# Optimization experiments

Hardware: AMD Instinct MI355X
Metric: run time of the kernel (lower is better)

## Reference

```python
import jax, jax.numpy as jnp
import numpy as np

EMBED_DIM = 2048
NUM_HEADS = 16
B, L = 1, 4096


def setup_inputs() -> dict:
    key = jax.random.key(0)
    ks = jax.random.split(key, 6)
    s = 1.0 / np.sqrt(EMBED_DIM)
    return {
        "hidden_states": jax.random.normal(ks[0], (B, L, EMBED_DIM), jnp.float32),
        "Wq": jax.random.normal(ks[1], (EMBED_DIM, EMBED_DIM), jnp.float32) * s,
        "bq": jnp.zeros((EMBED_DIM,), jnp.float32),
        "Wk": jax.random.normal(ks[2], (EMBED_DIM, EMBED_DIM), jnp.float32) * s,
        "bk": jnp.zeros((EMBED_DIM,), jnp.float32),
        "Wv": jax.random.normal(ks[3], (EMBED_DIM, EMBED_DIM), jnp.float32) * s,
        "bv": jnp.zeros((EMBED_DIM,), jnp.float32),
        "Wo": jax.random.normal(ks[4], (EMBED_DIM, EMBED_DIM), jnp.float32) * s,
        "bo": jnp.zeros((EMBED_DIM,), jnp.float32),
        "is_causal": 1,
    }


def reference(hidden_states, Wq, bq, Wk, bk, Wv, bv, Wo, bo, is_causal):
    Bc, Lc, D = hidden_states.shape
    H = NUM_HEADS
    Dh = D // H
    scale = Dh ** (-0.5)

    def proj(W, b):
        # torch Linear: x @ W.T + b; reshape to [B, H, L, Dh]
        y = jnp.einsum('bld,ed->ble', hidden_states, W) + b
        return y.reshape(Bc, Lc, H, Dh).transpose(0, 2, 1, 3)

    q = proj(Wq, bq)
    k = proj(Wk, bk)
    v = proj(Wv, bv)

    scores = jnp.einsum('bhqd,bhkd->bhqk', q, k) * scale  # [B,H,L,L]
    if is_causal:
        causal = jnp.triu(jnp.ones((Lc, Lc), dtype=bool), k=1)
        scores = jnp.where(causal, -jnp.inf, scores)
    w = jax.nn.softmax(scores, axis=-1)
    attn = jnp.einsum('bhqk,bhkd->bhqd', w, v)
    attn = attn.transpose(0, 2, 1, 3).reshape(Bc, Lc, D)
    return jnp.einsum('bld,ed->ble', attn, Wo) + bo
```

## Files before the change

kernel.cpp:

```cpp
#include <hip/hip_runtime.h>
#include <hip/hip_bf16.h>

typedef unsigned short u16;
typedef __attribute__((ext_vector_type(8))) short short8;
typedef __attribute__((ext_vector_type(4))) float f32x4;

#define L 4096
#define DMODEL 2048
#define NHEADS 16
#define DHEAD 128
#define QSCALE (0.08838834764831845f * 1.44269504088896340f)

__device__ __forceinline__ u16 f2bf(float f){
  union { float f; unsigned int i; } v; v.f = f;
  unsigned int u = v.i;
  u += 0x7fffu + ((u >> 16) & 1u);
  return (u16)(u >> 16);
}

__device__ __forceinline__ unsigned int cvtpk(float lo, float hi){
  unsigned int d;
  asm("v_cvt_pk_bf16_f32 %0, %1, %2" : "=v"(d) : "v"(lo), "v"(hi));
  return d;
}

__global__ void cast_kernel(const float* __restrict__ in, u16* __restrict__ out, int n){
  int stride = gridDim.x * blockDim.x * 4;
  for (int j = (blockIdx.x * blockDim.x + threadIdx.x) * 4; j < n; j += stride){
    float4 f = *reinterpret_cast<const float4*>(in + j);
    ushort4 o;
    o.x = f2bf(f.x); o.y = f2bf(f.y); o.z = f2bf(f.z); o.w = f2bf(f.w);
    *reinterpret_cast<ushort4*>(out + j) = o;
  }
}

__global__ void cast_w4_kernel(const float* __restrict__ w0, const float* __restrict__ w1,
                               const float* __restrict__ w2, const float* __restrict__ w3,
                               u16* __restrict__ o0, u16* __restrict__ o1,
                               u16* __restrict__ o2, u16* __restrict__ o3){
  const float* in = (blockIdx.y == 0) ? w0 : (blockIdx.y == 1) ? w1 : (blockIdx.y == 2) ? w2 : w3;
  u16* out = (blockIdx.y == 0) ? o0 : (blockIdx.y == 1) ? o1 : (blockIdx.y == 2) ? o2 : o3;
  const int n = DMODEL * DMODEL;
  int stride = gridDim.x * blockDim.x * 4;
  for (int j = (blockIdx.x * blockDim.x + threadIdx.x) * 4; j < n; j += stride){
    float4 f = *reinterpret_cast<const float4*>(in + j);
    ushort4 o;
    o.x = f2bf(f.x); o.y = f2bf(f.y); o.z = f2bf(f.z); o.w = f2bf(f.w);
    *reinterpret_cast<ushort4*>(out + j) = o;
  }
}

__device__ __forceinline__ void gl_lds16(void* lds, const void* g){
  __builtin_amdgcn_global_load_lds(
      (const __attribute__((address_space(1))) unsigned int*)g,
      (__attribute__((address_space(3))) unsigned int*)lds, 16, 0, 0);
}

#define GBUF (24576)

template<int MODE>
__global__ __launch_bounds__(512, 2) void gemm_bt(const u16* __restrict__ A, const u16* __restrict__ Bw,
                                                  const float* __restrict__ bias, void* __restrict__ outp,
                                                  float cscale){
  extern __shared__ u16 gsm[];
  const int tid = threadIdx.x;
  const int wid = tid >> 6, lane = tid & 63;
  const int wm = wid >> 2, wn = wid & 3;
  const int g = lane >> 4, r = lane & 15;
  const int bx = blockIdx.x, by = blockIdx.y;

  const int srow = tid >> 3;
  const int sc = ((tid & 7) * 16) ^ ((srow & 7) << 4);
  const u16* Ag = A  + ((size_t)(bx * 256) + srow) * DMODEL + (sc >> 1);
  const u16* Bg = Bw + ((size_t)(by * 128) + srow) * DMODEL + (sc >> 1);
  const int ldsw = wid * 1024;

  f32x4 acc[8][2];
  #pragma unroll
  for (int m = 0; m < 8; ++m){ acc[m][0] = (f32x4){0,0,0,0}; acc[m][1] = (f32x4){0,0,0,0}; }

  const int NK = DMODEL / 64;

  auto STAGE = [&](int b, int tk){
    char* ab = (char*)(gsm + b * GBUF);
    char* bb = (char*)(gsm + b * GBUF + 16384);
    const int ke = tk * 64;
    #pragma unroll
    for (int i = 0; i < 4; ++i)
      gl_lds16(ab + i * 8192 + ldsw, (const char*)(Ag + (size_t)i * 64 * DMODEL + ke));
    #pragma unroll
    for (int i = 0; i < 2; ++i)
      gl_lds16(bb + i * 8192 + ldsw, (const char*)(Bg + (size_t)i * 64 * DMODEL + ke));
  };

  STAGE(0, 0); STAGE(1, 1); STAGE(2, 2);

  int cur = 0;
  for (int t = 0; t < NK; ++t){
    if (t < NK - 2)      asm volatile("s_waitcnt vmcnt(12)" ::: "memory");
    else if (t == NK - 2) asm volatile("s_waitcnt vmcnt(6)"  ::: "memory");
    else                  asm volatile("s_waitcnt vmcnt(0)"  ::: "memory");
    __builtin_amdgcn_sched_barrier(0);
    __builtin_amdgcn_s_barrier();
    __builtin_amdgcn_sched_barrier(0);

    const char* ab = (const char*)(gsm + cur * GBUF);
    const char* bb = (const char*)(gsm + cur * GBUF + 16384);

    short8 af[8][2], bf[2][2];
    #pragma unroll
    for (int mt = 0; mt < 8; ++mt){
      const int ar = wm * 128 + mt * 16 + r;
      #pragma unroll
      for (int ks = 0; ks < 2; ++ks)
        af[mt][ks] = *reinterpret_cast<const short8*>(
            ab + ar * 128 + ((ks * 64 + g * 16) ^ ((ar & 7) << 4)));
    }
    #pragma unroll
    for (int nt = 0; nt < 2; ++nt){
      const int br = wn * 32 + nt * 16 + r;
      #pragma unroll
      for (int ks = 0; ks < 2; ++ks)
        bf[nt][ks] = *reinterpret_cast<const short8*>(
            bb + br * 128 + ((ks * 64 + g * 16) ^ ((br & 7) << 4)));
    }
    asm volatile("s_waitcnt lgkmcnt(0)" ::: "memory");
    __builtin_amdgcn_sched_barrier(0);
    __builtin_amdgcn_s_barrier();
    __builtin_amdgcn_sched_barrier(0);

    if (t + 3 < NK) STAGE(cur, t + 3);

    __builtin_amdgcn_s_setprio(1);
    #pragma unroll
    for (int mt = 0; mt < 8; ++mt)
      #pragma unroll
      for (int nt = 0; nt < 2; ++nt)
        #pragma unroll
        for (int ks = 0; ks < 2; ++ks)
          acc[mt][nt] = __builtin_amdgcn_mfma_f32_16x16x32_bf16(af[mt][ks], bf[nt][ks], acc[mt][nt], 0, 0, 0);
    __builtin_amdgcn_s_setprio(0);

    cur = (cur == 2) ? 0 : cur + 1;
  }

  #pragma unroll
  for (int nt = 0; nt < 2; ++nt){
    const int col = by * 128 + wn * 32 + nt * 16 + r;
    const float bv = bias[col];
    #pragma unroll
    for (int mt = 0; mt < 8; ++mt){
      #pragma unroll
      for (int qi = 0; qi < 4; ++qi){
        const int row = bx * 256 + wm * 128 + mt * 16 + g * 4 + qi;
        float c = acc[mt][nt][qi] + bv;
        if (MODE == 0){
          ((u16*)outp)[(size_t)(col >> 7) * (L * DHEAD) + (size_t)row * DHEAD + (col & 127)] = f2bf(c * cscale);
        } else if (MODE == 1){
          ((u16*)outp)[(size_t)(col >> 7) * (DHEAD * L) + (size_t)(col & 127) * L + row] = f2bf(c);
        } else {
          ((float*)outp)[(size_t)row * DMODEL + col] = c;
        }
      }
    }
  }
}


__device__ __forceinline__ void stage_K64(u16* buf, const u16* Kh, int kv0, int wid, int lane){
  #pragma unroll
  for (int i = 0; i < 4; ++i){
    int ib = (wid * 4 + i) * 1024;
    int off = ib + lane * 16;
    int row = off >> 8;
    int c = off & 255;
    int sc = c ^ ((row & 7) << 4);
    gl_lds16((char*)buf + ib, (const char*)(Kh + (size_t)(kv0 + row) * DHEAD) + sc);
  }
}

__device__ __forceinline__ void stage_V64(u16* buf, const u16* Vh, int kv0, int wid, int lane){
  #pragma unroll
  for (int i = 0; i < 4; ++i){
    int ib = (wid * 4 + i) * 1024;
    int off = ib + lane * 16;
    int row = off >> 7;
    int c = off & 127;
    int sc = c ^ ((row & 7) << 4);
    gl_lds16((char*)buf + ib, (const char*)(Vh + (size_t)row * L + kv0) + sc);
  }
}

__device__ __forceinline__ void sm_F(f32x4 (&s)[4], float &l, bool dg, int qrow,
                                     int kv0, int g, int r, char* Pw, int prow0){
  if (dg){
    #pragma unroll
    for (int cb = 0; cb < 4; ++cb){
      int kvb = kv0 + cb * 16 + g * 4;
      #pragma unroll
      for (int e = 0; e < 4; ++e)
        if (kvb + e > qrow) s[cb][e] = -1e30f;
    }
  }
  float rs = 0.f;
  uint2 pkv[4];
  #pragma unroll
  for (int cb = 0; cb < 4; ++cb){
    float p0 = __builtin_amdgcn_exp2f(s[cb][0]);
    float p1 = __builtin_amdgcn_exp2f(s[cb][1]);
    float p2 = __builtin_amdgcn_exp2f(s[cb][2]);
    float p3 = __builtin_amdgcn_exp2f(s[cb][3]);
    rs += (p0 + p1) + (p2 + p3);
    pkv[cb].x = cvtpk(p0, p1);
    pkv[cb].y = cvtpk(p2, p3);
  }
  rs += __shfl_xor(rs, 16);
  rs += __shfl_xor(rs, 32);
  l += rs;
  const int row = prow0 + r;
  char* base = Pw + row * 128;
  #pragma unroll
  for (int cb = 0; cb < 4; ++cb)
    *reinterpret_cast<uint2*>(base + ((cb * 32 + g * 8) ^ ((row & 7) << 4))) = pkv[cb];
}

__global__ __launch_bounds__(256, 2) void attn_kernel(const u16* __restrict__ Q, const u16* __restrict__ Km,
                                                      const u16* __restrict__ Vt, u16* __restrict__ Ob,
                                                      const int* __restrict__ is_causal_p){
  extern __shared__ u16 smem[];
  u16* Ks  = smem;
  u16* Vsm = smem + 16384;
  u16* Ps  = smem + 32768;

  const int lane = threadIdx.x & 63, wid = threadIdx.x >> 6;
  const int g = lane >> 4, r = lane & 15;

  int lg = (blockIdx.x & 7) * 64 + (blockIdx.x >> 3);
  int head = lg >> 5;
  int raw = lg & 31;
  int j = (head & 1) ? (31 - raw) : raw;
  const int jA = j, jB = 63 - j;
  const int causal = *is_causal_p;
  const int nt = causal ? (jB + 1) : 64;

  const u16* Qh = Q  + (size_t)head * L * DHEAD;
  const u16* Kh = Km + (size_t)head * L * DHEAD;
  const u16* Vh = Vt + (size_t)head * DHEAD * L;
  char* Pw = (char*)(Ps + wid * 2048);

  const int rowA = 64 * jA + wid * 16;
  const int rowB = 64 * jB + wid * 16;

  short8 qf[2][4];
  #pragma unroll
  for (int kb = 0; kb < 4; ++kb){
    qf[0][kb] = *reinterpret_cast<const short8*>(&Qh[(size_t)(rowA + r) * DHEAD + kb * 32 + g * 8]);
    qf[1][kb] = *reinterpret_cast<const short8*>(&Qh[(size_t)(rowB + r) * DHEAD + kb * 32 + g * 8]);
  }

  f32x4 o[2][8];
  #pragma unroll
  for (int m = 0; m < 2; ++m)
    #pragma unroll
    for (int db = 0; db < 8; ++db) o[m][db] = (f32x4){0.f, 0.f, 0.f, 0.f};
  float lA = 0.f, lB = 0.f;

  stage_K64(Ks,  Kh, 0, wid, lane);
  stage_V64(Vsm, Vh, 0, wid, lane);

  for (int t = 0; t < nt; ++t){
    const int kv0 = t * 64;
    const bool actA = (!causal) || (t <= jA);
    const bool dgA = causal && (t == jA);
    const bool dgB = causal && (t == jB);

    if (t + 1 < nt){
      stage_K64(Ks  + ((t + 1) & 1) * 8192, Kh, kv0 + 64, wid, lane);
      stage_V64(Vsm + ((t + 1) & 1) * 8192, Vh, kv0 + 64, wid, lane);
      asm volatile("s_waitcnt vmcnt(8)" ::: "memory");
    } else {
      asm volatile("s_waitcnt vmcnt(0)" ::: "memory");
    }
    __builtin_amdgcn_sched_barrier(0);
    __builtin_amdgcn_s_barrier();
    __builtin_amdgcn_sched_barrier(0);

    const char* Kb = (const char*)(Ks  + (t & 1) * 8192);
    const char* Vb = (const char*)(Vsm + (t & 1) * 8192);

    f32x4 s[2][4];
    #pragma unroll
    for (int m = 0; m < 2; ++m)
      #pragma unroll
      for (int cb = 0; cb < 4; ++cb) s[m][cb] = (f32x4){-16.f, -16.f, -16.f, -16.f};
    __builtin_amdgcn_s_setprio(1);
    #pragma unroll
    for (int cb = 0; cb < 4; ++cb){
      const int rr = cb * 16 + r;
      short8 kf[4];
      #pragma unroll
      for (int kb = 0; kb < 4; ++kb)
        kf[kb] = *reinterpret_cast<const short8*>(
            Kb + rr * 256 + ((kb * 64 + g * 16) ^ ((rr & 7) << 4)));
      if (actA){
        #pragma unroll
        for (int kb = 0; kb < 4; ++kb)
          s[0][cb] = __builtin_amdgcn_mfma_f32_16x16x32_bf16(kf[kb], qf[0][kb], s[0][cb], 0, 0, 0);
      }
      #pragma unroll
      for (int kb = 0; kb < 4; ++kb)
        s[1][cb] = __builtin_amdgcn_mfma_f32_16x16x32_bf16(kf[kb], qf[1][kb], s[1][cb], 0, 0, 0);
    }
    __builtin_amdgcn_s_setprio(0);

    if (actA) sm_F(s[0], lA, dgA, rowA + r, kv0, g, r, Pw, 0);
    sm_F(s[1], lB, dgB, rowB + r, kv0, g, r, Pw, 16);

    asm volatile("s_waitcnt lgkmcnt(0)" ::: "memory");
    __builtin_amdgcn_sched_barrier(0);

    __builtin_amdgcn_s_setprio(1);
    #pragma unroll
    for (int st = 0; st < 2; ++st){
      short8 pa0, pa1;
      if (actA)
        pa0 = *reinterpret_cast<const short8*>(
            Pw + r * 128 + ((st * 64 + g * 16) ^ ((r & 7) << 4)));
      pa1 = *reinterpret_cast<const short8*>(
          Pw + (16 + r) * 128 + ((st * 64 + g * 16) ^ ((r & 7) << 4)));
      #pragma unroll
      for (int db = 0; db < 8; ++db){
        const int rv = db * 16 + r;
        short8 vf = *reinterpret_cast<const short8*>(
            Vb + rv * 128 + ((st * 32 + g * 8) * 2 ^ ((rv & 7) << 4)));
        if (actA)
          o[0][db] = __builtin_amdgcn_mfma_f32_16x16x32_bf16(pa0, vf, o[0][db], 0, 0, 0);
        o[1][db] = __builtin_amdgcn_mfma_f32_16x16x32_bf16(pa1, vf, o[1][db], 0, 0, 0);
      }
    }
    __builtin_amdgcn_s_setprio(0);
    __builtin_amdgcn_sched_barrier(0);
    __builtin_amdgcn_s_barrier();
    __builtin_amdgcn_sched_barrier(0);
  }

  #pragma unroll
  for (int m = 0; m < 2; ++m){
    const int rbase = m ? rowB : rowA;
    const float lv = m ? lB : lA;
    float lb[4];
    #pragma unroll
    for (int qi = 0; qi < 4; ++qi) lb[qi] = __shfl(lv, g * 4 + qi);
    #pragma unroll
    for (int db = 0; db < 8; ++db)
      #pragma unroll
      for (int qi = 0; qi < 4; ++qi){
        float val = o[m][db][qi] / lb[qi];
        int qrow = rbase + g * 4 + qi;
        Ob[(size_t)qrow * DMODEL + head * DHEAD + db * 16 + r] = f2bf(val);
      }
  }
}

extern "C" void kernel_launch(void* const* d_in, const int* in_sizes, int n_in,
                              void* d_out, int out_size, void* d_ws, size_t ws_size,
                              hipStream_t stream){
  const float* X  = (const float*)d_in[0];
  const float* Wq = (const float*)d_in[1];
  const float* bq = (const float*)d_in[2];
  const float* Wk = (const float*)d_in[3];
  const float* bk = (const float*)d_in[4];
  const float* Wv = (const float*)d_in[5];
  const float* bv = (const float*)d_in[6];
  const float* Wo = (const float*)d_in[7];
  const float* bo = (const float*)d_in[8];
  const int*   isc = (const int*)d_in[9];

  char* ws = (char*)d_ws;
  u16* Xb  = (u16*)(ws);
  u16* Qb  = (u16*)(ws + 16777216);
  u16* Kb  = (u16*)(ws + 33554432);
  u16* Vtb = (u16*)(ws + 50331648);
  u16* Wqb = (u16*)(ws + 67108864);
  u16* Wkb = (u16*)(ws + 75497472);
  u16* Wvb = (u16*)(ws + 83886080);
  u16* Wob = (u16*)(ws + 92274688);
  u16* Ob  = Xb;

  (void)hipFuncSetAttribute(reinterpret_cast<const void*>(attn_kernel),
                            hipFuncAttributeMaxDynamicSharedMemorySize, 81920);
  (void)hipFuncSetAttribute(reinterpret_cast<const void*>(gemm_bt<0>),
                            hipFuncAttributeMaxDynamicSharedMemorySize, 147456);
  (void)hipFuncSetAttribute(reinterpret_cast<const void*>(gemm_bt<1>),
                            hipFuncAttributeMaxDynamicSharedMemorySize, 147456);
  (void)hipFuncSetAttribute(reinterpret_cast<const void*>(gemm_bt<2>),
                            hipFuncAttributeMaxDynamicSharedMemorySize, 147456);

  cast_kernel<<<2048, 256, 0, stream>>>(X, Xb, L * DMODEL);
  cast_w4_kernel<<<dim3(1024, 4), 256, 0, stream>>>(Wq, Wk, Wv, Wo, Wqb, Wkb, Wvb, Wob);

  dim3 gg(16, 16);
  gemm_bt<0><<<gg, 512, 147456, stream>>>(Xb, Wqb, bq, Qb, QSCALE);
  gemm_bt<0><<<gg, 512, 147456, stream>>>(Xb, Wkb, bk, Kb, 1.0f);
  gemm_bt<1><<<gg, 512, 147456, stream>>>(Xb, Wvb, bv, Vtb, 1.0f);

  attn_kernel<<<512, 256, 81920, stream>>>(Qb, Kb, Vtb, Ob, isc);

  gemm_bt<2><<<gg, 512, 147456, stream>>>(Ob, Wob, bo, d_out, 1.0f);
}
```

Measured before the change: 302.9 us.

## Merge QKV GEMMs into one launch and cut pipeline barriers

Folds the three Q/K/V projection GEMMs into one kernel with a 16x48 grid, selecting weights, bias, scale and output layout per block row, so the GPU sees one larger wave of work instead of three serial launches. Both GEMMs now use a single barrier per k-step with stage distance two over a triple buffer, instead of a second barrier before the prefetch. The attention kernel moves its single barrier to the top of each iteration after vmcnt(0), drops the trailing barrier, and issues all V fragment loads before the P loads. Fewer barriers reduce stalls but leave less load-latency slack, since the GEMM waits with vmcnt(6) and attention waits with vmcnt(0) before issuing the next prefetch.

Measured after the change: 299.7 us. No clear change (-1.1%).

```diff
diff --git a/kernel.cpp b/kernel.cpp
--- a/kernel.cpp
+++ b/kernel.cpp
@@ -58,10 +58,113 @@
 
 #define GBUF (24576)
 
-template<int MODE>
-__global__ __launch_bounds__(512, 2) void gemm_bt(const u16* __restrict__ A, const u16* __restrict__ Bw,
-                                                  const float* __restrict__ bias, void* __restrict__ outp,
-                                                  float cscale){
+__global__ __launch_bounds__(512, 2) void gemm_qkv(const u16* __restrict__ A,
+    const u16* __restrict__ Wq, const u16* __restrict__ Wk, const u16* __restrict__ Wv,
+    const float* __restrict__ bq, const float* __restrict__ bk, const float* __restrict__ bv,
+    u16* __restrict__ Qb, u16* __restrict__ Kb, u16* __restrict__ Vtb){
+  extern __shared__ u16 gsm[];
+  const int tid = threadIdx.x;
+  const int wid = tid >> 6, lane = tid & 63;
+  const int wm = wid >> 2, wn = wid & 3;
+  const int g = lane >> 4, r = lane & 15;
+  const int bx = blockIdx.x;
+  const int sel = blockIdx.y >> 4;
+  const int byl = blockIdx.y & 15;
+
+  const u16* W      = (sel == 0) ? Wq : (sel == 1) ? Wk : Wv;
+  const float* bias = (sel == 0) ? bq : (sel == 1) ? bk : bv;
+  const float cscale = (sel == 0) ? QSCALE : 1.0f;
+
+  const int srow = tid >> 3;
+  const int sc = ((tid & 7) * 16) ^ ((srow & 7) << 4);
+  const u16* Ag = A + ((size_t)(bx * 256) + srow) * DMODEL + (sc >> 1);
+  const u16* Bg = W + ((size_t)(byl * 128) + srow) * DMODEL + (sc >> 1);
+  const int ldsw = wid * 1024;
+
+  f32x4 acc[8][2];
+  #pragma unroll
+  for (int m = 0; m < 8; ++m){ acc[m][0] = (f32x4){0,0,0,0}; acc[m][1] = (f32x4){0,0,0,0}; }
+
+  const int NK = DMODEL / 64;
+
+  auto STAGE = [&](int b, int tk){
+    char* ab = (char*)(gsm + b * GBUF);
+    char* bb = (char*)(gsm + b * GBUF + 16384);
+    const int ke = tk * 64;
+    #pragma unroll
+    for (int i = 0; i < 4; ++i)
+      gl_lds16(ab + i * 8192 + ldsw, (const char*)(Ag + (size_t)i * 64 * DMODEL + ke));
+    #pragma unroll
+    for (int i = 0; i < 2; ++i)
+      gl_lds16(bb + i * 8192 + ldsw, (const char*)(Bg + (size_t)i * 64 * DMODEL + ke));
+  };
+
+  STAGE(0, 0); STAGE(1, 1);
+
+  for (int t = 0; t < NK; ++t){
+    if (t < NK - 1) asm volatile("s_waitcnt vmcnt(6)" ::: "memory");
+    else            asm volatile("s_waitcnt vmcnt(0)" ::: "memory");
+    __builtin_amdgcn_sched_barrier(0);
+    __builtin_amdgcn_s_barrier();
+    __builtin_amdgcn_sched_barrier(0);
+
+    if (t + 2 < NK) STAGE((t + 2) % 3, t + 2);
+
+    const char* ab = (const char*)(gsm + (t % 3) * GBUF);
+    const char* bb = (const char*)(gsm + (t % 3) * GBUF + 16384);
+
+    short8 af[8][2], bf[2][2];
+    #pragma unroll
+    for (int mt = 0; mt < 8; ++mt){
+      const int ar = wm * 128 + mt * 16 + r;
+      #pragma unroll
+      for (int ks = 0; ks < 2; ++ks)
+        af[mt][ks] = *reinterpret_cast<const short8*>(
+            ab + ar * 128 + ((ks * 64 + g * 16) ^ ((ar & 7) << 4)));
+    }
+    #pragma unroll
+    for (int nt = 0; nt < 2; ++nt){
+      const int br = wn * 32 + nt * 16 + r;
+      #pragma unroll
+      for (int ks = 0; ks < 2; ++ks)
+        bf[nt][ks] = *reinterpret_cast<const short8*>(
+            bb + br * 128 + ((ks * 64 + g * 16) ^ ((br & 7) << 4)));
+    }
+
+    __builtin_amdgcn_s_setprio(1);
+    #pragma unroll
+    for (int mt = 0; mt < 8; ++mt)
+      #pragma unroll
+      for (int nt = 0; nt < 2; ++nt)
+        #pragma unroll
+        for (int ks = 0; ks < 2; ++ks)
+          acc[mt][nt] = __builtin_amdgcn_mfma_f32_16x16x32_bf16(af[mt][ks], bf[nt][ks], acc[mt][nt], 0, 0, 0);
+    __builtin_amdgcn_s_setprio(0);
+  }
+
+  #pragma unroll
+  for (int nt = 0; nt < 2; ++nt){
+    const int col = byl * 128 + wn * 32 + nt * 16 + r;
+    const float bv = bias[col];
+    #pragma unroll
+    for (int mt = 0; mt < 8; ++mt){
+      #pragma unroll
+      for (int qi = 0; qi < 4; ++qi){
+        const int row = bx * 256 + wm * 128 + mt * 16 + g * 4 + qi;
+        const u16 hb = f2bf((acc[mt][nt][qi] + bv) * cscale);
+        if (sel < 2){
+          u16* outp = (sel == 0) ? Qb : Kb;
+          outp[(size_t)(col >> 7) * (L * DHEAD) + (size_t)row * DHEAD + (col & 127)] = hb;
+        } else {
+          Vtb[(size_t)(col >> 7) * (DHEAD * L) + (size_t)(col & 127) * L + row] = hb;
+        }
+      }
+    }
+  }
+}
+
+__global__ __launch_bounds__(512, 2) void gemm_o(const u16* __restrict__ A, const u16* __restrict__ W,
+                                                 const float* __restrict__ bias, float* __restrict__ outp){
   extern __shared__ u16 gsm[];
   const int tid = threadIdx.x;
   const int wid = tid >> 6, lane = tid & 63;
@@ -71,8 +174,8 @@
 
   const int srow = tid >> 3;
   const int sc = ((tid & 7) * 16) ^ ((srow & 7) << 4);
-  const u16* Ag = A  + ((size_t)(bx * 256) + srow) * DMODEL + (sc >> 1);
-  const u16* Bg = Bw + ((size_t)(by * 128) + srow) * DMODEL + (sc >> 1);
+  const u16* Ag = A + ((size_t)(bx * 256) + srow) * DMODEL + (sc >> 1);
+  const u16* Bg = W + ((size_t)(by * 128) + srow) * DMODEL + (sc >> 1);
   const int ldsw = wid * 1024;
 
   f32x4 acc[8][2];
@@ -93,19 +196,19 @@
       gl_lds16(bb + i * 8192 + ldsw, (const char*)(Bg + (size_t)i * 64 * DMODEL + ke));
   };
 
-  STAGE(0, 0); STAGE(1, 1); STAGE(2, 2);
-
-  int cur = 0;
+  STAGE(0, 0); STAGE(1, 1);
+
   for (int t = 0; t < NK; ++t){
-    if (t < NK - 2)      asm volatile("s_waitcnt vmcnt(12)" ::: "memory");
-    else if (t == NK - 2) asm volatile("s_waitcnt vmcnt(6)"  ::: "memory");
-    else                  asm volatile("s_waitcnt vmcnt(0)"  ::: "memory");
+    if (t < NK - 1) asm volatile("s_waitcnt vmcnt(6)" ::: "memory");
+    else            asm volatile("s_waitcnt vmcnt(0)" ::: "memory");
     __builtin_amdgcn_sched_barrier(0);
     __builtin_amdgcn_s_barrier();
     __builtin_amdgcn_sched_barrier(0);
 
-    const char* ab = (const char*)(gsm + cur * GBUF);
-    const char* bb = (const char*)(gsm + cur * GBUF + 16384);
+    if (t + 2 < NK) STAGE((t + 2) % 3, t + 2);
+
+    const char* ab = (const char*)(gsm + (t % 3) * GBUF);
+    const char* bb = (const char*)(gsm + (t % 3) * GBUF + 16384);
 
     short8 af[8][2], bf[2][2];
     #pragma unroll
@@ -124,12 +227,6 @@
         bf[nt][ks] = *reinterpret_cast<const short8*>(
             bb + br * 128 + ((ks * 64 + g * 16) ^ ((br & 7) << 4)));
     }
-    asm volatile("s_waitcnt lgkmcnt(0)" ::: "memory");
-    __builtin_amdgcn_sched_barrier(0);
-    __builtin_amdgcn_s_barrier();
-    __builtin_amdgcn_sched_barrier(0);
-
-    if (t + 3 < NK) STAGE(cur, t + 3);
 
     __builtin_amdgcn_s_setprio(1);
     #pragma unroll
@@ -140,8 +237,6 @@
         for (int ks = 0; ks < 2; ++ks)
           acc[mt][nt] = __builtin_amdgcn_mfma_f32_16x16x32_bf16(af[mt][ks], bf[nt][ks], acc[mt][nt], 0, 0, 0);
     __builtin_amdgcn_s_setprio(0);
-
-    cur = (cur == 2) ? 0 : cur + 1;
   }
 
   #pragma unroll
@@ -153,14 +248,7 @@
       #pragma unroll
       for (int qi = 0; qi < 4; ++qi){
         const int row = bx * 256 + wm * 128 + mt * 16 + g * 4 + qi;
-        float c = acc[mt][nt][qi] + bv;
-        if (MODE == 0){
-          ((u16*)outp)[(size_t)(col >> 7) * (L * DHEAD) + (size_t)row * DHEAD + (col & 127)] = f2bf(c * cscale);
-        } else if (MODE == 1){
-          ((u16*)outp)[(size_t)(col >> 7) * (DHEAD * L) + (size_t)(col & 127) * L + row] = f2bf(c);
-        } else {
-          ((float*)outp)[(size_t)row * DMODEL + col] = c;
-        }
+        outp[(size_t)row * DMODEL + col] = acc[mt][nt][qi] + bv;
       }
     }
   }
@@ -274,16 +362,15 @@
     const bool dgA = causal && (t == jA);
     const bool dgB = causal && (t == jB);
 
+    asm volatile("s_waitcnt vmcnt(0)" ::: "memory");
+    __builtin_amdgcn_sched_barrier(0);
+    __builtin_amdgcn_s_barrier();
+    __builtin_amdgcn_sched_barrier(0);
+
     if (t + 1 < nt){
       stage_K64(Ks  + ((t + 1) & 1) * 8192, Kh, kv0 + 64, wid, lane);
       stage_V64(Vsm + ((t + 1) & 1) * 8192, Vh, kv0 + 64, wid, lane);
-      asm volatile("s_waitcnt vmcnt(8)" ::: "memory");
-    } else {
-      asm volatile("s_waitcnt vmcnt(0)" ::: "memory");
-    }
-    __builtin_amdgcn_sched_barrier(0);
-    __builtin_amdgcn_s_barrier();
-    __builtin_amdgcn_sched_barrier(0);
+    }
 
     const char* Kb = (const char*)(Ks  + (t & 1) * 8192);
     const char* Vb = (const char*)(Vsm + (t & 1) * 8192);
@@ -316,12 +403,20 @@
     if (actA) sm_F(s[0], lA, dgA, rowA + r, kv0, g, r, Pw, 0);
     sm_F(s[1], lB, dgB, rowB + r, kv0, g, r, Pw, 16);
 
-    asm volatile("s_waitcnt lgkmcnt(0)" ::: "memory");
-    __builtin_amdgcn_sched_barrier(0);
-
     __builtin_amdgcn_s_setprio(1);
     #pragma unroll
     for (int st = 0; st < 2; ++st){
+      short8 vf[8];
+      #pragma unroll
+      for (int db = 0; db < 8; ++db){
+        const int rv = db * 16 + r;
+        vf[db] = *reinterpret_cast<const short8*>(
+            Vb + rv * 128 + (((st * 32 + g * 8) * 2) ^ ((rv & 7) << 4)));
+      }
+      if (st == 0){
+        asm volatile("s_waitcnt lgkmcnt(0)" ::: "memory");
+        __builtin_amdgcn_sched_barrier(0);
+      }
       short8 pa0, pa1;
       if (actA)
         pa0 = *reinterpret_cast<const short8*>(
@@ -330,18 +425,12 @@
           Pw + (16 + r) * 128 + ((st * 64 + g * 16) ^ ((r & 7) << 4)));
       #pragma unroll
       for (int db = 0; db < 8; ++db){
-        const int rv = db * 16 + r;
-        short8 vf = *reinterpret_cast<const short8*>(
-            Vb + rv * 128 + ((st * 32 + g * 8) * 2 ^ ((rv & 7) << 4)));
         if (actA)
-          o[0][db] = __builtin_amdgcn_mfma_f32_16x16x32_bf16(pa0, vf, o[0][db], 0, 0, 0);
-        o[1][db] = __builtin_amdgcn_mfma_f32_16x16x32_bf16(pa1, vf, o[1][db], 0, 0, 0);
+          o[0][db] = __builtin_amdgcn_mfma_f32_16x16x32_bf16(pa0, vf[db], o[0][db], 0, 0, 0);
+        o[1][db] = __builtin_amdgcn_mfma_f32_16x16x32_bf16(pa1, vf[db], o[1][db], 0, 0, 0);
       }
     }
     __builtin_amdgcn_s_setprio(0);
-    __builtin_amdgcn_sched_barrier(0);
-    __builtin_amdgcn_s_barrier();
-    __builtin_amdgcn_sched_barrier(0);
   }
 
   #pragma unroll
@@ -389,22 +478,17 @@
 
   (void)hipFuncSetAttribute(reinterpret_cast<const void*>(attn_kernel),
                             hipFuncAttributeMaxDynamicSharedMemorySize, 81920);
-  (void)hipFuncSetAttribute(reinterpret_cast<const void*>(gemm_bt<0>),
+  (void)hipFuncSetAttribute(reinterpret_cast<const void*>(gemm_qkv),
                             hipFuncAttributeMaxDynamicSharedMemorySize, 147456);
-  (void)hipFuncSetAttribute(reinterpret_cast<const void*>(gemm_bt<1>),
-                            hipFuncAttributeMaxDynamicSharedMemorySize, 147456);
-  (void)hipFuncSetAttribute(reinterpret_cast<const void*>(gemm_bt<2>),
+  (void)hipFuncSetAttribute(reinterpret_cast<const void*>(gemm_o),
                             hipFuncAttributeMaxDynamicSharedMemorySize, 147456);
 
   cast_kernel<<<2048, 256, 0, stream>>>(X, Xb, L * DMODEL);
   cast_w4_kernel<<<dim3(1024, 4), 256, 0, stream>>>(Wq, Wk, Wv, Wo, Wqb, Wkb, Wvb, Wob);
 
-  dim3 gg(16, 16);
-  gemm_bt<0><<<gg, 512, 147456, stream>>>(Xb, Wqb, bq, Qb, QSCALE);
-  gemm_bt<0><<<gg, 512, 147456, stream>>>(Xb, Wkb, bk, Kb, 1.0f);
-  gemm_bt<1><<<gg, 512, 147456, stream>>>(Xb, Wvb, bv, Vtb, 1.0f);
+  gemm_qkv<<<dim3(16, 48), 512, 147456, stream>>>(Xb, Wqb, Wkb, Wvb, bq, bk, bv, Qb, Kb, Vtb);
 
   attn_kernel<<<512, 256, 81920, stream>>>(Qb, Kb, Vtb, Ob, isc);
 
-  gemm_bt<2><<<gg, 512, 147456, stream>>>(Ob, Wob, bo, d_out, 1.0f);
-}
+  gemm_o<<<dim3(16, 16), 512, 147456, stream>>>(Ob, Wob, bo, (float*)d_out);
+}
```

## Fuse QKV GEMMs into one launch, shrink K-tile and retune pipelines

Applied to the files above, without the earlier changes.

The three Q/K/V projection launches are merged into one kernel with a 48-row grid that selects the weight, bias and output layout per block. The GEMM core moves to a 32-wide K tile with three smaller LDS buffers, a single barrier per iteration, and 4 blocks per CU instead of 2. The XOR swizzle on the GEMM LDS tiles is dropped, which may add bank conflicts. The attention loop is also restructured: one barrier at the top of each iteration, and all V fragments loaded before the P·V MFMAs to overlap LDS latency.

Measured after the change: 308.3 us. Within noise of the previous version (+1.8%).

```diff
diff --git a/kernel.cpp b/kernel.cpp
--- a/kernel.cpp
+++ b/kernel.cpp
@@ -56,92 +56,78 @@
       (__attribute__((address_space(3))) unsigned int*)lds, 16, 0, 0);
 }
 
-#define GBUF (24576)
-
-template<int MODE>
-__global__ __launch_bounds__(512, 2) void gemm_bt(const u16* __restrict__ A, const u16* __restrict__ Bw,
-                                                  const float* __restrict__ bias, void* __restrict__ outp,
-                                                  float cscale){
-  extern __shared__ u16 gsm[];
+#define GBUF 12288
+
+template<int OUT_QKV>
+__device__ __forceinline__ void gemm_core(const u16* __restrict__ A, const u16* __restrict__ W,
+                                          const float* __restrict__ bias, void* __restrict__ out0,
+                                          void* __restrict__ out1, float cscale, int sel,
+                                          int bx, int by, u16* gsm){
   const int tid = threadIdx.x;
   const int wid = tid >> 6, lane = tid & 63;
   const int wm = wid >> 2, wn = wid & 3;
   const int g = lane >> 4, r = lane & 15;
-  const int bx = blockIdx.x, by = blockIdx.y;
-
-  const int srow = tid >> 3;
-  const int sc = ((tid & 7) * 16) ^ ((srow & 7) << 4);
-  const u16* Ag = A  + ((size_t)(bx * 256) + srow) * DMODEL + (sc >> 1);
-  const u16* Bg = Bw + ((size_t)(by * 128) + srow) * DMODEL + (sc >> 1);
+
+  const int srow = tid >> 2;
+  const int scol = (tid & 3) * 8;
+  const u16* Ag = A + ((size_t)(bx * 256) + srow) * DMODEL + scol;
+  const u16* Bg = W + ((size_t)(by * 128) + srow) * DMODEL + scol;
   const int ldsw = wid * 1024;
 
   f32x4 acc[8][2];
   #pragma unroll
   for (int m = 0; m < 8; ++m){ acc[m][0] = (f32x4){0,0,0,0}; acc[m][1] = (f32x4){0,0,0,0}; }
 
-  const int NK = DMODEL / 64;
+  const int NK = DMODEL / 32;
 
   auto STAGE = [&](int b, int tk){
     char* ab = (char*)(gsm + b * GBUF);
-    char* bb = (char*)(gsm + b * GBUF + 16384);
-    const int ke = tk * 64;
-    #pragma unroll
-    for (int i = 0; i < 4; ++i)
-      gl_lds16(ab + i * 8192 + ldsw, (const char*)(Ag + (size_t)i * 64 * DMODEL + ke));
-    #pragma unroll
-    for (int i = 0; i < 2; ++i)
-      gl_lds16(bb + i * 8192 + ldsw, (const char*)(Bg + (size_t)i * 64 * DMODEL + ke));
+    char* bb = (char*)(gsm + b * GBUF + 8192);
+    const int ke = tk * 32;
+    gl_lds16(ab +        ldsw, (const char*)(Ag + ke));
+    gl_lds16(ab + 8192 + ldsw, (const char*)(Ag + (size_t)128 * DMODEL + ke));
+    gl_lds16(bb +        ldsw, (const char*)(Bg + ke));
   };
 
-  STAGE(0, 0); STAGE(1, 1); STAGE(2, 2);
+  STAGE(0, 0); STAGE(1, 1);
 
   int cur = 0;
   for (int t = 0; t < NK; ++t){
-    if (t < NK - 2)      asm volatile("s_waitcnt vmcnt(12)" ::: "memory");
-    else if (t == NK - 2) asm volatile("s_waitcnt vmcnt(6)"  ::: "memory");
-    else                  asm volatile("s_waitcnt vmcnt(0)"  ::: "memory");
+    if (t < NK - 1) asm volatile("s_waitcnt vmcnt(3)" ::: "memory");
+    else            asm volatile("s_waitcnt vmcnt(0)" ::: "memory");
     __builtin_amdgcn_sched_barrier(0);
     __builtin_amdgcn_s_barrier();
     __builtin_amdgcn_sched_barrier(0);
 
+    if (t + 2 < NK){
+      int nb = cur + 2; if (nb >= 3) nb -= 3;
+      STAGE(nb, t + 2);
+    }
+
     const char* ab = (const char*)(gsm + cur * GBUF);
-    const char* bb = (const char*)(gsm + cur * GBUF + 16384);
-
-    short8 af[8][2], bf[2][2];
+    const char* bb = (const char*)(gsm + cur * GBUF + 8192);
+
+    short8 af[8], bf[2];
     #pragma unroll
     for (int mt = 0; mt < 8; ++mt){
       const int ar = wm * 128 + mt * 16 + r;
-      #pragma unroll
-      for (int ks = 0; ks < 2; ++ks)
-        af[mt][ks] = *reinterpret_cast<const short8*>(
-            ab + ar * 128 + ((ks * 64 + g * 16) ^ ((ar & 7) << 4)));
+      af[mt] = *reinterpret_cast<const short8*>(ab + ar * 64 + g * 16);
     }
     #pragma unroll
     for (int nt = 0; nt < 2; ++nt){
       const int br = wn * 32 + nt * 16 + r;
-      #pragma unroll
-      for (int ks = 0; ks < 2; ++ks)
-        bf[nt][ks] = *reinterpret_cast<const short8*>(
-            bb + br * 128 + ((ks * 64 + g * 16) ^ ((br & 7) << 4)));
-    }
-    asm volatile("s_waitcnt lgkmcnt(0)" ::: "memory");
-    __builtin_amdgcn_sched_barrier(0);
-    __builtin_amdgcn_s_barrier();
-    __builtin_amdgcn_sched_barrier(0);
-
-    if (t + 3 < NK) STAGE(cur, t + 3);
+      bf[nt] = *reinterpret_cast<const short8*>(bb + br * 64 + g * 16);
+    }
 
     __builtin_amdgcn_s_setprio(1);
     #pragma unroll
     for (int mt = 0; mt < 8; ++mt)
       #pragma unroll
       for (int nt = 0; nt < 2; ++nt)
-        #pragma unroll
-        for (int ks = 0; ks < 2; ++ks)
-          acc[mt][nt] = __builtin_amdgcn_mfma_f32_16x16x32_bf16(af[mt][ks], bf[nt][ks], acc[mt][nt], 0, 0, 0);
+        acc[mt][nt] = __builtin_amdgcn_mfma_f32_16x16x32_bf16(af[mt], bf[nt], acc[mt][nt], 0, 0, 0);
     __builtin_amdgcn_s_setprio(0);
 
-    cur = (cur == 2) ? 0 : cur + 1;
+    ++cur; if (cur == 3) cur = 0;
   }
 
   #pragma unroll
@@ -153,17 +139,39 @@
       #pragma unroll
       for (int qi = 0; qi < 4; ++qi){
         const int row = bx * 256 + wm * 128 + mt * 16 + g * 4 + qi;
-        float c = acc[mt][nt][qi] + bv;
-        if (MODE == 0){
-          ((u16*)outp)[(size_t)(col >> 7) * (L * DHEAD) + (size_t)row * DHEAD + (col & 127)] = f2bf(c * cscale);
-        } else if (MODE == 1){
-          ((u16*)outp)[(size_t)(col >> 7) * (DHEAD * L) + (size_t)(col & 127) * L + row] = f2bf(c);
+        if (OUT_QKV){
+          const u16 hb = f2bf((acc[mt][nt][qi] + bv) * cscale);
+          if (sel < 2){
+            ((u16*)out0)[(size_t)(col >> 7) * (L * DHEAD) + (size_t)row * DHEAD + (col & 127)] = hb;
+          } else {
+            ((u16*)out1)[(size_t)(col >> 7) * (DHEAD * L) + (size_t)(col & 127) * L + row] = hb;
+          }
         } else {
-          ((float*)outp)[(size_t)row * DMODEL + col] = c;
+          ((float*)out0)[(size_t)row * DMODEL + col] = acc[mt][nt][qi] + bv;
         }
       }
     }
   }
+}
+
+__global__ __launch_bounds__(512, 4) void gemm_qkv(const u16* __restrict__ A,
+    const u16* __restrict__ Wq, const u16* __restrict__ Wk, const u16* __restrict__ Wv,
+    const float* __restrict__ bq, const float* __restrict__ bk, const float* __restrict__ bv,
+    u16* __restrict__ Qb, u16* __restrict__ Kb, u16* __restrict__ Vtb){
+  extern __shared__ u16 gsm[];
+  const int sel = blockIdx.y >> 4;
+  const int byl = blockIdx.y & 15;
+  const u16* W      = (sel == 0) ? Wq : (sel == 1) ? Wk : Wv;
+  const float* bias = (sel == 0) ? bq : (sel == 1) ? bk : bv;
+  const float cscale = (sel == 0) ? QSCALE : 1.0f;
+  void* o0 = (sel == 0) ? (void*)Qb : (void*)Kb;
+  gemm_core<1>(A, W, bias, o0, (void*)Vtb, cscale, sel, blockIdx.x, byl, gsm);
+}
+
+__global__ __launch_bounds__(512, 4) void gemm_o(const u16* __restrict__ A, const u16* __restrict__ W,
+                                                 const float* __restrict__ bias, float* __restrict__ outp){
+  extern __shared__ u16 gsm[];
+  gemm_core<0>(A, W, bias, (void*)outp, nullptr, 1.0f, 0, blockIdx.y, gsm ? blockIdx.x : 0, gsm);
 }
 
 
@@ -274,16 +282,15 @@
     const bool dgA = causal && (t == jA);
     const bool dgB = causal && (t == jB);
 
+    asm volatile("s_waitcnt vmcnt(0)" ::: "memory");
+    __builtin_amdgcn_sched_barrier(0);
+    __builtin_amdgcn_s_barrier();
+    __builtin_amdgcn_sched_barrier(0);
+
     if (t + 1 < nt){
       stage_K64(Ks  + ((t + 1) & 1) * 8192, Kh, kv0 + 64, wid, lane);
       stage_V64(Vsm + ((t + 1) & 1) * 8192, Vh, kv0 + 64, wid, lane);
-      asm volatile("s_waitcnt vmcnt(8)" ::: "memory");
-    } else {
-      asm volatile("s_waitcnt vmcnt(0)" ::: "memory");
-    }
-    __builtin_amdgcn_sched_barrier(0);
-    __builtin_amdgcn_s_barrier();
-    __builtin_amdgcn_sched_barrier(0);
+    }
 
     const char* Kb = (const char*)(Ks  + (t & 1) * 8192);
     const char* Vb = (const char*)(Vsm + (t & 1) * 8192);
@@ -316,12 +323,20 @@
     if (actA) sm_F(s[0], lA, dgA, rowA + r, kv0, g, r, Pw, 0);
     sm_F(s[1], lB, dgB, rowB + r, kv0, g, r, Pw, 16);
 
-    asm volatile("s_waitcnt lgkmcnt(0)" ::: "memory");
-    __builtin_amdgcn_sched_barrier(0);
-
     __builtin_amdgcn_s_setprio(1);
     #pragma unroll
     for (int st = 0; st < 2; ++st){
+      short8 vf[8];
+      #pragma unroll
+      for (int db = 0; db < 8; ++db){
+        const int rv = db * 16 + r;
+        vf[db] = *reinterpret_cast<const short8*>(
+            Vb + rv * 128 + (((st * 32 + g * 8) * 2) ^ ((rv & 7) << 4)));
+      }
+      if (st == 0){
+        asm volatile("s_waitcnt lgkmcnt(0)" ::: "memory");
+        __builtin_amdgcn_sched_barrier(0);
+      }
       short8 pa0, pa1;
       if (actA)
         pa0 = *reinterpret_cast<const short8*>(
@@ -330,18 +345,12 @@
           Pw + (16 + r) * 128 + ((st * 64 + g * 16) ^ ((r & 7) << 4)));
       #pragma unroll
       for (int db = 0; db < 8; ++db){
-        const int rv = db * 16 + r;
-        short8 vf = *reinterpret_cast<const short8*>(
-            Vb + rv * 128 + ((st * 32 + g * 8) * 2 ^ ((rv & 7) << 4)));
         if (actA)
-          o[0][db] = __builtin_amdgcn_mfma_f32_16x16x32_bf16(pa0, vf, o[0][db], 0, 0, 0);
-        o[1][db] = __builtin_amdgcn_mfma_f32_16x16x32_bf16(pa1, vf, o[1][db], 0, 0, 0);
+          o[0][db] = __builtin_amdgcn_mfma_f32_16x16x32_bf16(pa0, vf[db], o[0][db], 0, 0, 0);
+        o[1][db] = __builtin_amdgcn_mfma_f32_16x16x32_bf16(pa1, vf[db], o[1][db], 0, 0, 0);
       }
     }
     __builtin_amdgcn_s_setprio(0);
-    __builtin_amdgcn_sched_barrier(0);
-    __builtin_amdgcn_s_barrier();
-    __builtin_amdgcn_sched_barrier(0);
   }
 
   #pragma unroll
@@ -389,22 +398,17 @@
 
   (void)hipFuncSetAttribute(reinterpret_cast<const void*>(attn_kernel),
                             hipFuncAttributeMaxDynamicSharedMemorySize, 81920);
-  (void)hipFuncSetAttribute(reinterpret_cast<const void*>(gemm_bt<0>),
-                            hipFuncAttributeMaxDynamicSharedMemorySize, 147456);
-  (void)hipFuncSetAttribute(reinterpret_cast<const void*>(gemm_bt<1>),
-                            hipFuncAttributeMaxDynamicSharedMemorySize, 147456);
-  (void)hipFuncSetAttribute(reinterpret_cast<const void*>(gemm_bt<2>),
-                            hipFuncAttributeMaxDynamicSharedMemorySize, 147456);
+  (void)hipFuncSetAttribute(reinterpret_cast<const void*>(gemm_qkv),
+                            hipFuncAttributeMaxDynamicSharedMemorySize, 73728);
+  (void)hipFuncSetAttribute(reinterpret_cast<const void*>(gemm_o),
+                            hipFuncAttributeMaxDynamicSharedMemorySize, 73728);
 
   cast_kernel<<<2048, 256, 0, stream>>>(X, Xb, L * DMODEL);
   cast_w4_kernel<<<dim3(1024, 4), 256, 0, stream>>>(Wq, Wk, Wv, Wo, Wqb, Wkb, Wvb, Wob);
 
-  dim3 gg(16, 16);
-  gemm_bt<0><<<gg, 512, 147456, stream>>>(Xb, Wqb, bq, Qb, QSCALE);
-  gemm_bt<0><<<gg, 512, 147456, stream>>>(Xb, Wkb, bk, Kb, 1.0f);
-  gemm_bt<1><<<gg, 512, 147456, stream>>>(Xb, Wvb, bv, Vtb, 1.0f);
+  gemm_qkv<<<dim3(16, 48), 512, 73728, stream>>>(Xb, Wqb, Wkb, Wvb, bq, bk, bv, Qb, Kb, Vtb);
 
   attn_kernel<<<512, 256, 81920, stream>>>(Qb, Kb, Vtb, Ob, isc);
 
-  gemm_bt<2><<<gg, 512, 147456, stream>>>(Ob, Wob, bo, d_out, 1.0f);
-}
+  gemm_o<<<dim3(16, 16), 512, 73728, stream>>>(Ob, Wob, bo, (float*)d_out);
+}
```
